# Kernel optimization log

Measured on AMD Instinct MI355X. Metric: run time of the kernel, lower is better.

Reference implementation:

```python
import jax, jax.numpy as jnp
import numpy as np

N = 50000   # nodes
E = 600000  # edges (before self loops)
D = 128     # in = hidden = out channels
EPS = 1e-5


def setup_inputs() -> dict:
    key = jax.random.key(0)
    ks = jax.random.split(key, 12)
    s = 1.0 / np.sqrt(D)
    inp = {
        "x": jax.random.normal(ks[0], (N, D), jnp.float32),
        "edge_index": jax.random.randint(ks[1], (2, E), 0, N, dtype=jnp.int64),
        "W1": jax.random.normal(ks[2], (D, D), jnp.float32) * s,
        "b1": jnp.zeros((D,), jnp.float32),
        "g1": jnp.ones((D,), jnp.float32),
        "be1": jnp.zeros((D,), jnp.float32),
        "W2": jax.random.normal(ks[3], (D, D), jnp.float32) * s,
        "b2": jnp.zeros((D,), jnp.float32),
        "g2": jnp.ones((D,), jnp.float32),
        "be2": jnp.zeros((D,), jnp.float32),
        "W3": jax.random.normal(ks[4], (D, D), jnp.float32) * s,
        "b3": jnp.zeros((D,), jnp.float32),
    }
    return inp


def _layer_norm(h, g, b):
    mu = jnp.mean(h, axis=-1, keepdims=True)
    var = jnp.mean(jnp.square(h - mu), axis=-1, keepdims=True)
    return (h - mu) * jax.lax.rsqrt(var + EPS) * g + b


def _gcn_layer(h, src, dst, ew, W, b, fill):
    # PyG gcn_norm: append internal self loops with weight `fill`
    loop = jnp.arange(N, dtype=src.dtype)
    s = jnp.concatenate([src, loop])
    d = jnp.concatenate([dst, loop])
    w = jnp.concatenate([ew, jnp.full((N,), fill, h.dtype)])
    deg = jax.ops.segment_sum(w, d, num_segments=N)
    dinv = jnp.where(deg > 0, jax.lax.rsqrt(deg), 0.0)
    norm = dinv[s] * w * dinv[d]  # [E_tot]
    hw = h @ W                    # [N, D]
    out = jax.ops.segment_sum(norm[:, None] * hw[s], d, num_segments=N)
    return out + b


def reference(x, edge_index, W1, b1, g1, be1, W2, b2, g2, be2, W3, b3):
    # outer add_self_loops with edge_weight = 1 (edge_attr is None path)
    loop = jnp.arange(N, dtype=edge_index.dtype)
    src = jnp.concatenate([edge_index[0], loop])
    dst = jnp.concatenate([edge_index[1], loop])
    ew = jnp.ones((E + N,), x.dtype)

    residual = x
    h = _gcn_layer(x, src, dst, ew, W1, b1, 2.0)   # improved=True
    h = jax.nn.relu(_layer_norm(h, g1, be1))
    h = _gcn_layer(h, src, dst, ew, W2, b2, 2.0)   # improved=True
    h = jax.nn.relu(_layer_norm(h, g2, be2))
    h = _gcn_layer(h, src, dst, ew, W3, b3, 1.0)   # improved=False
    return h + residual
```

## Files before the change

### kernel.cpp

```cpp
#include <hip/hip_runtime.h>
#include <hip/hip_bf16.h>
#include <cstdint>

#define N_NODES 50000
#define N_EDGES 600000
#define DCH     128
#define LN_EPS  1e-5f
#define SCAN_BLOCKS 196
#define CSR_CAP 1000000

typedef __attribute__((ext_vector_type(8))) __bf16 bf16x8;
typedef __attribute__((ext_vector_type(4))) float  f32x4;

__device__ inline unsigned short f2bf(float f) {
    unsigned int b; __builtin_memcpy(&b, &f, 4);
    b = b + 0x7fffu + ((b >> 16) & 1u);
    return (unsigned short)(b >> 16);
}
__device__ inline float bf_lo(unsigned int u) {
    unsigned int t = u << 16; float f; __builtin_memcpy(&f, &t, 4); return f;
}
__device__ inline float bf_hi(unsigned int u) {
    unsigned int t = u & 0xffff0000u; float f; __builtin_memcpy(&f, &t, 4); return f;
}

__global__ void detect_k(const int* __restrict__ ei, int* __restrict__ flag) {
    __shared__ int bad;
    if (threadIdx.x == 0) bad = 0;
    __syncthreads();
    const long long* e64 = (const long long*)ei;
    long long v = e64[threadIdx.x];
    long long w = e64[300000 + threadIdx.x];
    if (v < 0 || v >= N_NODES || w < 0 || w >= N_NODES) bad = 1;
    __syncthreads();
    if (threadIdx.x == 0) *flag = (bad == 0) ? 1 : 0;
}

__device__ inline int edge_at(const int* __restrict__ ei, int is64, long long idx) {
    long long v = is64 ? ((const long long*)ei)[idx] : (long long)ei[idx];
    if (v < 0) v = 0;
    if (v >= N_NODES) v = N_NODES - 1;
    return (int)v;
}


__global__ void count_k(const int* __restrict__ ei, const int* __restrict__ flag,
                        int* __restrict__ cnt) {
    int e = blockIdx.x * 256 + threadIdx.x;
    if (e < N_EDGES) {
        int d = edge_at(ei, *flag, (long long)N_EDGES + e);
        atomicAdd(&cnt[d], 1);
    }
}

__global__ void scan_block_k(const int* __restrict__ cnt, int* __restrict__ row_start,
                             int* __restrict__ bsums) {
    __shared__ int sm[256];
    int t = threadIdx.x;
    int i = blockIdx.x * 256 + t;
    int v = (i < N_NODES) ? ((cnt[i] + 7) & ~7) : 0;
    sm[t] = v; __syncthreads();
    #pragma unroll
    for (int off = 1; off < 256; off <<= 1) {
        int x = (t >= off) ? sm[t - off] : 0;
        __syncthreads();
        sm[t] += x;
        __syncthreads();
    }
    if (i < N_NODES) row_start[i] = sm[t] - v;
    if (t == 255)    bsums[blockIdx.x] = sm[255];
}

__global__ void scan_top_k(int* __restrict__ bsums) {
    __shared__ int sm[256];
    int t = threadIdx.x;
    int v = (t < SCAN_BLOCKS) ? bsums[t] : 0;
    sm[t] = v; __syncthreads();
    #pragma unroll
    for (int off = 1; off < 256; off <<= 1) {
        int x = (t >= off) ? sm[t - off] : 0;
        __syncthreads();
        sm[t] += x;
        __syncthreads();
    }
    if (t < SCAN_BLOCKS) bsums[t] = sm[t] - v;
}

__global__ void finalize_k(const int* __restrict__ cnt, int* __restrict__ row_start,
                           int* __restrict__ cursor, const int* __restrict__ bsums,
                           float* __restrict__ dinv2, float* __restrict__ dinv1) {
    int i = blockIdx.x * 256 + threadIdx.x;
    if (i >= N_NODES) return;
    int rs = row_start[i] + bsums[blockIdx.x];
    row_start[i] = rs;
    cursor[i]    = rs;
    float c = (float)cnt[i];
    dinv2[i] = rsqrtf(c + 3.0f);
    dinv1[i] = rsqrtf(c + 2.0f);
}

__global__ void pad_fill_k(int* __restrict__ csr) {
    int i = blockIdx.x * 256 + threadIdx.x;
    if (i < CSR_CAP) csr[i] = N_NODES;
}

__global__ void fill_k(const int* __restrict__ ei, const int* __restrict__ flag,
                       int* __restrict__ cursor, int* __restrict__ csr) {
    int e = blockIdx.x * 256 + threadIdx.x;
    if (e >= N_EDGES) return;
    int is64 = *flag;
    int s = edge_at(ei, is64, e);
    int d = edge_at(ei, is64, (long long)N_EDGES + e);
    int pos = atomicAdd(&cursor[d], 1);
    csr[pos] = s;
}

__global__ void cvt_x_k(const float* __restrict__ x, const float* __restrict__ dinv2,
                        unsigned short* __restrict__ xbf) {
    int idx = blockIdx.x * 256 + threadIdx.x;
    int node = idx >> 5;
    if (node > N_NODES) return;
    int co = (idx & 31) * 4;
    uint2 r;
    if (node == N_NODES) {
        r.x = 0u; r.y = 0u;
    } else {
        float4 v = *(const float4*)(x + (size_t)node * DCH + co);
        float d = dinv2[node];
        r.x = ((unsigned int)f2bf(v.y * d) << 16) | (unsigned int)f2bf(v.x * d);
        r.y = ((unsigned int)f2bf(v.w * d) << 16) | (unsigned int)f2bf(v.z * d);
    }
    *(uint2*)(xbf + (size_t)node * DCH + co) = r;
}

__global__ void transpose_k(const float* __restrict__ W1,
                            const float* __restrict__ W2,
                            const float* __restrict__ W3,
                            unsigned short* __restrict__ Wt) {
    int t = blockIdx.x * 256 + threadIdx.x;
    int mat = t >> 14;
    int o = t & 16383;
    int n = o >> 7, k = o & 127;
    const float* W = (mat == 0) ? W1 : ((mat == 1) ? W2 : W3);
    Wt[t] = f2bf(W[k * 128 + n]);
}


__global__ __launch_bounds__(256) void agg_k(
        const unsigned short* __restrict__ hs, unsigned short* __restrict__ out,
        const int* __restrict__ row_start, const int* __restrict__ cnt,
        const int* __restrict__ csr, const float* __restrict__ dinv, float fillp1) {
    int lane = threadIdx.x & 63;
    int node = blockIdx.x * 4 + (threadIdx.x >> 6);
    float di = dinv[node];
    int rs = row_start[node];
    int pc = (cnt[node] + 7) & ~7;
    const unsigned int* hp = (const unsigned int*)hs + lane;
    float a00 = 0.f, a01 = 0.f, a10 = 0.f, a11 = 0.f;
    float a20 = 0.f, a21 = 0.f, a30 = 0.f, a31 = 0.f;
    float a40 = 0.f, a41 = 0.f, a50 = 0.f, a51 = 0.f;
    float a60 = 0.f, a61 = 0.f, a70 = 0.f, a71 = 0.f;
    for (int i = 0; i < pc; i += 8) {
        int e0 = csr[rs+i+0], e1 = csr[rs+i+1], e2 = csr[rs+i+2], e3 = csr[rs+i+3];
        int e4 = csr[rs+i+4], e5 = csr[rs+i+5], e6 = csr[rs+i+6], e7 = csr[rs+i+7];
        unsigned int u0 = hp[(size_t)e0 * 64];
        unsigned int u1 = hp[(size_t)e1 * 64];
        unsigned int u2 = hp[(size_t)e2 * 64];
        unsigned int u3 = hp[(size_t)e3 * 64];
        unsigned int u4 = hp[(size_t)e4 * 64];
        unsigned int u5 = hp[(size_t)e5 * 64];
        unsigned int u6 = hp[(size_t)e6 * 64];
        unsigned int u7 = hp[(size_t)e7 * 64];
        a00 += bf_lo(u0); a01 += bf_hi(u0);
        a10 += bf_lo(u1); a11 += bf_hi(u1);
        a20 += bf_lo(u2); a21 += bf_hi(u2);
        a30 += bf_lo(u3); a31 += bf_hi(u3);
        a40 += bf_lo(u4); a41 += bf_hi(u4);
        a50 += bf_lo(u5); a51 += bf_hi(u5);
        a60 += bf_lo(u6); a61 += bf_hi(u6);
        a70 += bf_lo(u7); a71 += bf_hi(u7);
    }
    float s0 = ((a00 + a10) + (a20 + a30)) + ((a40 + a50) + (a60 + a70));
    float s1 = ((a01 + a11) + (a21 + a31)) + ((a41 + a51) + (a61 + a71));
    unsigned int us = hp[(size_t)node * 64];
    s0 = di * (s0 + fillp1 * bf_lo(us));
    s1 = di * (s1 + fillp1 * bf_hi(us));
    unsigned int res = ((unsigned int)f2bf(s1) << 16) | (unsigned int)f2bf(s0);
    *((unsigned int*)out + (size_t)node * 64 + lane) = res;
}


template<int MODE>
__global__ __launch_bounds__(256) void gemm_k(
        const unsigned short* __restrict__ A,
        const unsigned short* __restrict__ Wt,
        const float* __restrict__ bias,
        const float* __restrict__ gamma,
        const float* __restrict__ beta,
        const float* __restrict__ dnext,
        const float* __restrict__ resid,
        unsigned short* __restrict__ out_bf,
        float* __restrict__ out_f) {
    int lane = threadIdx.x & 63;
    int wv   = threadIdx.x >> 6;
    int r0   = (blockIdx.x * 4 + wv) * 32;
    int m = lane & 15, q = lane >> 4;

    bf16x8 afr[2][4];
    #pragma unroll
    for (int mt = 0; mt < 2; mt++) {
        int arow = r0 + mt * 16 + m; if (arow >= N_NODES) arow = N_NODES - 1;
        const unsigned short* ap = A + (size_t)arow * DCH + q * 8;
        #pragma unroll
        for (int kt = 0; kt < 4; kt++) afr[mt][kt] = *(const bf16x8*)(ap + kt * 32);
    }

    f32x4 acc[2][8];
    #pragma unroll
    for (int nt = 0; nt < 8; nt++) {
        f32x4 c0 = {0.f,0.f,0.f,0.f}, c1 = {0.f,0.f,0.f,0.f};
        const unsigned short* bp = Wt + (size_t)(nt * 16 + m) * DCH + q * 8;
        #pragma unroll
        for (int kt = 0; kt < 4; kt++) {
            bf16x8 bfr = *(const bf16x8*)(bp + kt * 32);
            c0 = __builtin_amdgcn_mfma_f32_16x16x32_bf16(afr[0][kt], bfr, c0, 0, 0, 0);
            c1 = __builtin_amdgcn_mfma_f32_16x16x32_bf16(afr[1][kt], bfr, c1, 0, 0, 0);
        }
        acc[0][nt] = c0; acc[1][nt] = c1;
    }

    float bv[8];
    #pragma unroll
    for (int nt = 0; nt < 8; nt++) bv[nt] = bias[nt * 16 + m];

    if (MODE == 0) {
        float gv[8], bev[8];
        #pragma unroll
        for (int nt = 0; nt < 8; nt++) { gv[nt] = gamma[nt*16+m]; bev[nt] = beta[nt*16+m]; }
        #pragma unroll
        for (int mt = 0; mt < 2; mt++) {
            #pragma unroll
            for (int nt = 0; nt < 8; nt++)
                #pragma unroll
                for (int r = 0; r < 4; r++) acc[mt][nt][r] += bv[nt];
            #pragma unroll
            for (int r = 0; r < 4; r++) {
                float s = 0.f, qs = 0.f;
                #pragma unroll
                for (int nt = 0; nt < 8; nt++) { float v = acc[mt][nt][r]; s += v; qs += v*v; }
                #pragma unroll
                for (int msk = 1; msk < 16; msk <<= 1) {
                    s  += __shfl_xor(s,  msk, 16);
                    qs += __shfl_xor(qs, msk, 16);
                }
                float mean = s * (1.f / 128.f);
                float var  = fmaxf(qs * (1.f / 128.f) - mean * mean, 0.f);
                float rstd = rsqrtf(var + LN_EPS);
                int row = r0 + mt * 16 + q * 4 + r;
                if (row < N_NODES) {
                    float dscale = dnext[row];
                    #pragma unroll
                    for (int nt = 0; nt < 8; nt++) {
                        float v = (acc[mt][nt][r] - mean) * rstd * gv[nt] + bev[nt];
                        v = fmaxf(v, 0.f) * dscale;
                        out_bf[(size_t)row * DCH + nt * 16 + m] = f2bf(v);
                    }
                }
            }
        }
    } else {
        #pragma unroll
        for (int mt = 0; mt < 2; mt++)
            #pragma unroll
            for (int r = 0; r < 4; r++) {
                int row = r0 + mt * 16 + q * 4 + r;
                if (row < N_NODES) {
                    #pragma unroll
                    for (int nt = 0; nt < 8; nt++) {
                        float v = acc[mt][nt][r] + bv[nt]
                                + resid[(size_t)row * DCH + nt * 16 + m];
                        out_f[(size_t)row * DCH + nt * 16 + m] = v;
                    }
                }
            }
    }
}


extern "C" void kernel_launch(void* const* d_in, const int* in_sizes, int n_in,
                              void* d_out, int out_size, void* d_ws, size_t ws_size,
                              hipStream_t stream) {
    const float* x   = (const float*)d_in[0];
    const int*   ei  = (const int*)d_in[1];
    const float* W1  = (const float*)d_in[2];
    const float* b1  = (const float*)d_in[3];
    const float* g1  = (const float*)d_in[4];
    const float* be1 = (const float*)d_in[5];
    const float* W2  = (const float*)d_in[6];
    const float* b2  = (const float*)d_in[7];
    const float* g2  = (const float*)d_in[8];
    const float* be2 = (const float*)d_in[9];
    const float* W3  = (const float*)d_in[10];
    const float* b3  = (const float*)d_in[11];
    float* out = (float*)d_out;

    char* p = (char*)d_ws;
    auto alloc = [&](size_t bytes) -> void* {
        void* r = (void*)p; p += (bytes + 255) & ~(size_t)255; return r;
    };
    int*   eflag     = (int*)  alloc(256);
    int*   cnt       = (int*)  alloc((size_t)N_NODES * 4);
    int*   row_start = (int*)  alloc((size_t)N_NODES * 4);
    int*   cursor    = (int*)  alloc((size_t)N_NODES * 4);
    int*   bsums     = (int*)  alloc(256 * 4);
    float* dinv2     = (float*)alloc((size_t)N_NODES * 4);
    float* dinv1     = (float*)alloc((size_t)N_NODES * 4);
    int*   csr       = (int*)  alloc((size_t)CSR_CAP * 4);
    unsigned short* Wt   = (unsigned short*)alloc((size_t)3 * 128 * 128 * 2);
    unsigned short* aggb = (unsigned short*)alloc((size_t)N_NODES * DCH * 2);
    unsigned short* xbf  = (unsigned short*)alloc((size_t)(N_NODES + 1) * DCH * 2);
    unsigned short* hbuf = (unsigned short*)alloc((size_t)(N_NODES + 1) * DCH * 2);

    hipMemsetAsync(cnt, 0, (size_t)N_NODES * 4, stream);
    hipMemsetAsync(hbuf + (size_t)N_NODES * DCH, 0, DCH * 2, stream);
    detect_k<<<1, 256, 0, stream>>>(ei, eflag);
    count_k<<<(N_EDGES + 255) / 256, 256, 0, stream>>>(ei, eflag, cnt);
    scan_block_k<<<SCAN_BLOCKS, 256, 0, stream>>>(cnt, row_start, bsums);
    scan_top_k<<<1, 256, 0, stream>>>(bsums);
    finalize_k<<<SCAN_BLOCKS, 256, 0, stream>>>(cnt, row_start, cursor, bsums, dinv2, dinv1);
    pad_fill_k<<<(CSR_CAP + 255) / 256, 256, 0, stream>>>(csr);
    fill_k<<<(N_EDGES + 255) / 256, 256, 0, stream>>>(ei, eflag, cursor, csr);
    cvt_x_k<<<((N_NODES + 1) * 32 + 255) / 256, 256, 0, stream>>>(x, dinv2, xbf);
    transpose_k<<<192, 256, 0, stream>>>(W1, W2, W3, Wt);

    const int G_BLOCKS = (N_NODES + 127) / 128;

    agg_k<<<N_NODES / 4, 256, 0, stream>>>(xbf, aggb, row_start, cnt, csr, dinv2, 3.0f);
    gemm_k<0><<<G_BLOCKS, 256, 0, stream>>>(aggb, Wt, b1, g1, be1, dinv2, nullptr, hbuf, nullptr);
    agg_k<<<N_NODES / 4, 256, 0, stream>>>(hbuf, aggb, row_start, cnt, csr, dinv2, 3.0f);
    gemm_k<0><<<G_BLOCKS, 256, 0, stream>>>(aggb, Wt + 16384, b2, g2, be2, dinv1, nullptr, hbuf, nullptr);
    agg_k<<<N_NODES / 4, 256, 0, stream>>>(hbuf, aggb, row_start, cnt, csr, dinv1, 2.0f);
    gemm_k<1><<<G_BLOCKS, 256, 0, stream>>>(aggb, Wt + 32768, b3, nullptr, nullptr, nullptr, x, nullptr, out);
}
```

Measured before the change: 310.5 us.

## Split bf16 feature buffers into four column slices for cache-local gathers

```diff
diff --git a/kernel.cpp b/kernel.cpp
--- a/kernel.cpp
+++ b/kernel.cpp
@@ -8,6 +8,7 @@
 #define LN_EPS  1e-5f
 #define SCAN_BLOCKS 196
 #define CSR_CAP 1000000
+#define SLICE_N (N_NODES + 1)
 
 typedef __attribute__((ext_vector_type(8))) __bf16 bf16x8;
 typedef __attribute__((ext_vector_type(4))) float  f32x4;
@@ -121,6 +122,7 @@
     int node = idx >> 5;
     if (node > N_NODES) return;
     int co = (idx & 31) * 4;
+    int slice = co >> 5, off = co & 31;
     uint2 r;
     if (node == N_NODES) {
         r.x = 0u; r.y = 0u;
@@ -130,7 +132,12 @@
         r.x = ((unsigned int)f2bf(v.y * d) << 16) | (unsigned int)f2bf(v.x * d);
         r.y = ((unsigned int)f2bf(v.w * d) << 16) | (unsigned int)f2bf(v.z * d);
     }
-    *(uint2*)(xbf + (size_t)node * DCH + co) = r;
+    *(uint2*)(xbf + ((size_t)slice * SLICE_N + node) * 32 + off) = r;
+}
+
+__global__ void zero_sent_k(unsigned short* __restrict__ hbuf) {
+    int t = threadIdx.x;
+    if (t < 128) hbuf[((size_t)(t >> 5) * SLICE_N + N_NODES) * 32 + (t & 31)] = 0;
 }
 
 __global__ void transpose_k(const float* __restrict__ W1,
@@ -147,46 +154,39 @@
 
 
 __global__ __launch_bounds__(256) void agg_k(
-        const unsigned short* __restrict__ hs, unsigned short* __restrict__ out,
+        const unsigned short* __restrict__ hs, unsigned short* __restrict__ outb,
         const int* __restrict__ row_start, const int* __restrict__ cnt,
         const int* __restrict__ csr, const float* __restrict__ dinv, float fillp1) {
-    int lane = threadIdx.x & 63;
-    int node = blockIdx.x * 4 + (threadIdx.x >> 6);
+    int slice = blockIdx.x & 3;
+    int grp   = blockIdx.x >> 2;
+    int wv    = threadIdx.x >> 6;
+    int node  = grp * 4 + wv;
+    int lane  = threadIdx.x & 63;
+    int g = lane >> 4, c = lane & 15;
+    const unsigned int* hp = (const unsigned int*)hs + (size_t)slice * SLICE_N * 16;
     float di = dinv[node];
     int rs = row_start[node];
     int pc = (cnt[node] + 7) & ~7;
-    const unsigned int* hp = (const unsigned int*)hs + lane;
-    float a00 = 0.f, a01 = 0.f, a10 = 0.f, a11 = 0.f;
-    float a20 = 0.f, a21 = 0.f, a30 = 0.f, a31 = 0.f;
-    float a40 = 0.f, a41 = 0.f, a50 = 0.f, a51 = 0.f;
-    float a60 = 0.f, a61 = 0.f, a70 = 0.f, a71 = 0.f;
+    float a0 = 0.f, a1 = 0.f, b0 = 0.f, b1 = 0.f;
     for (int i = 0; i < pc; i += 8) {
-        int e0 = csr[rs+i+0], e1 = csr[rs+i+1], e2 = csr[rs+i+2], e3 = csr[rs+i+3];
-        int e4 = csr[rs+i+4], e5 = csr[rs+i+5], e6 = csr[rs+i+6], e7 = csr[rs+i+7];
-        unsigned int u0 = hp[(size_t)e0 * 64];
-        unsigned int u1 = hp[(size_t)e1 * 64];
-        unsigned int u2 = hp[(size_t)e2 * 64];
-        unsigned int u3 = hp[(size_t)e3 * 64];
-        unsigned int u4 = hp[(size_t)e4 * 64];
-        unsigned int u5 = hp[(size_t)e5 * 64];
-        unsigned int u6 = hp[(size_t)e6 * 64];
-        unsigned int u7 = hp[(size_t)e7 * 64];
-        a00 += bf_lo(u0); a01 += bf_hi(u0);
-        a10 += bf_lo(u1); a11 += bf_hi(u1);
-        a20 += bf_lo(u2); a21 += bf_hi(u2);
-        a30 += bf_lo(u3); a31 += bf_hi(u3);
-        a40 += bf_lo(u4); a41 += bf_hi(u4);
-        a50 += bf_lo(u5); a51 += bf_hi(u5);
-        a60 += bf_lo(u6); a61 += bf_hi(u6);
-        a70 += bf_lo(u7); a71 += bf_hi(u7);
-    }
-    float s0 = ((a00 + a10) + (a20 + a30)) + ((a40 + a50) + (a60 + a70));
-    float s1 = ((a01 + a11) + (a21 + a31)) + ((a41 + a51) + (a61 + a71));
-    unsigned int us = hp[(size_t)node * 64];
-    s0 = di * (s0 + fillp1 * bf_lo(us));
-    s1 = di * (s1 + fillp1 * bf_hi(us));
-    unsigned int res = ((unsigned int)f2bf(s1) << 16) | (unsigned int)f2bf(s0);
-    *((unsigned int*)out + (size_t)node * 64 + lane) = res;
+        int ea = __builtin_nontemporal_load(&csr[rs + i + g]);
+        int eb = __builtin_nontemporal_load(&csr[rs + i + 4 + g]);
+        unsigned int ua = hp[(size_t)ea * 16 + c];
+        unsigned int ub = hp[(size_t)eb * 16 + c];
+        a0 += bf_lo(ua); a1 += bf_hi(ua);
+        b0 += bf_lo(ub); b1 += bf_hi(ub);
+    }
+    a0 += b0; a1 += b1;
+    a0 += __shfl_xor(a0, 16); a0 += __shfl_xor(a0, 32);
+    a1 += __shfl_xor(a1, 16); a1 += __shfl_xor(a1, 32);
+    if (g == 0) {
+        unsigned int us = hp[(size_t)node * 16 + c];
+        float s0 = di * (a0 + fillp1 * bf_lo(us));
+        float s1 = di * (a1 + fillp1 * bf_hi(us));
+        unsigned int res = ((unsigned int)f2bf(s1) << 16) | (unsigned int)f2bf(s0);
+        __builtin_nontemporal_store(res,
+            (unsigned int*)outb + (size_t)slice * SLICE_N * 16 + (size_t)node * 16 + c);
+    }
 }
 
 
@@ -210,9 +210,10 @@
     #pragma unroll
     for (int mt = 0; mt < 2; mt++) {
         int arow = r0 + mt * 16 + m; if (arow >= N_NODES) arow = N_NODES - 1;
-        const unsigned short* ap = A + (size_t)arow * DCH + q * 8;
-        #pragma unroll
-        for (int kt = 0; kt < 4; kt++) afr[mt][kt] = *(const bf16x8*)(ap + kt * 32);
+        #pragma unroll
+        for (int kt = 0; kt < 4; kt++)
+            afr[mt][kt] = __builtin_nontemporal_load(
+                (const bf16x8*)(A + ((size_t)kt * SLICE_N + arow) * 32 + q * 8));
     }
 
     f32x4 acc[2][8];
@@ -263,7 +264,9 @@
                     for (int nt = 0; nt < 8; nt++) {
                         float v = (acc[mt][nt][r] - mean) * rstd * gv[nt] + bev[nt];
                         v = fmaxf(v, 0.f) * dscale;
-                        out_bf[(size_t)row * DCH + nt * 16 + m] = f2bf(v);
+                        __builtin_nontemporal_store(f2bf(v),
+                            out_bf + ((size_t)(nt >> 1) * SLICE_N + row) * 32
+                                   + (nt & 1) * 16 + m);
                     }
                 }
             }
@@ -317,12 +320,12 @@
     float* dinv1     = (float*)alloc((size_t)N_NODES * 4);
     int*   csr       = (int*)  alloc((size_t)CSR_CAP * 4);
     unsigned short* Wt   = (unsigned short*)alloc((size_t)3 * 128 * 128 * 2);
-    unsigned short* aggb = (unsigned short*)alloc((size_t)N_NODES * DCH * 2);
-    unsigned short* xbf  = (unsigned short*)alloc((size_t)(N_NODES + 1) * DCH * 2);
-    unsigned short* hbuf = (unsigned short*)alloc((size_t)(N_NODES + 1) * DCH * 2);
+    unsigned short* aggb = (unsigned short*)alloc((size_t)4 * SLICE_N * 32 * 2);
+    unsigned short* xbf  = (unsigned short*)alloc((size_t)4 * SLICE_N * 32 * 2);
+    unsigned short* hbuf = (unsigned short*)alloc((size_t)4 * SLICE_N * 32 * 2);
 
     hipMemsetAsync(cnt, 0, (size_t)N_NODES * 4, stream);
-    hipMemsetAsync(hbuf + (size_t)N_NODES * DCH, 0, DCH * 2, stream);
+    zero_sent_k<<<1, 256, 0, stream>>>(hbuf);
     detect_k<<<1, 256, 0, stream>>>(ei, eflag);
     count_k<<<(N_EDGES + 255) / 256, 256, 0, stream>>>(ei, eflag, cnt);
     scan_block_k<<<SCAN_BLOCKS, 256, 0, stream>>>(cnt, row_start, bsums);
@@ -333,12 +336,13 @@
     cvt_x_k<<<((N_NODES + 1) * 32 + 255) / 256, 256, 0, stream>>>(x, dinv2, xbf);
     transpose_k<<<192, 256, 0, stream>>>(W1, W2, W3, Wt);
 
+    const int A_BLOCKS = (N_NODES / 4) * 4;
     const int G_BLOCKS = (N_NODES + 127) / 128;
 
-    agg_k<<<N_NODES / 4, 256, 0, stream>>>(xbf, aggb, row_start, cnt, csr, dinv2, 3.0f);
+    agg_k<<<A_BLOCKS, 256, 0, stream>>>(xbf, aggb, row_start, cnt, csr, dinv2, 3.0f);
     gemm_k<0><<<G_BLOCKS, 256, 0, stream>>>(aggb, Wt, b1, g1, be1, dinv2, nullptr, hbuf, nullptr);
-    agg_k<<<N_NODES / 4, 256, 0, stream>>>(hbuf, aggb, row_start, cnt, csr, dinv2, 3.0f);
+    agg_k<<<A_BLOCKS, 256, 0, stream>>>(hbuf, aggb, row_start, cnt, csr, dinv2, 3.0f);
     gemm_k<0><<<G_BLOCKS, 256, 0, stream>>>(aggb, Wt + 16384, b2, g2, be2, dinv1, nullptr, hbuf, nullptr);
-    agg_k<<<N_NODES / 4, 256, 0, stream>>>(hbuf, aggb, row_start, cnt, csr, dinv1, 2.0f);
+    agg_k<<<A_BLOCKS, 256, 0, stream>>>(hbuf, aggb, row_start, cnt, csr, dinv1, 2.0f);
     gemm_k<1><<<G_BLOCKS, 256, 0, stream>>>(aggb, Wt + 32768, b3, nullptr, nullptr, nullptr, x, nullptr, out);
 }
```

Result: slower. 489.0 us (+57.5%).
